# Kernel optimization log

Hardware: AMD Instinct MI355X
Metric: run time of the kernel (lower is better)

## Reference

```python
import jax, jax.numpy as jnp
import numpy as np

B, K, C, HEADS, R, N, FF = 8, 512, 256, 8, 4, 64, 1024
HT = 2 * R + 1  # rel-pos table side = 9


def layer_norm(x, g, b, eps=1e-5):
    mu = jnp.mean(x, axis=-1, keepdims=True)
    var = jnp.var(x, axis=-1, keepdims=True)
    return (x - mu) * jax.lax.rsqrt(var + eps) * g + b


def grid_sample_table(table, grid):
    """Bilinear grid_sample, align_corners=True, zeros padding.
    table: [heads, H, W] (batch-expanded in torch, identical per batch)
    grid:  [b, k, n, 2] in [-1, 1]  ->  out [b, heads, k, n]
    """
    heads, H, W = table.shape
    gx = (grid[..., 0] + 1.0) * 0.5 * (W - 1)
    gy = (grid[..., 1] + 1.0) * 0.5 * (H - 1)
    x0 = jnp.floor(gx); y0 = jnp.floor(gy)
    x1 = x0 + 1.0;      y1 = y0 + 1.0
    wx1 = gx - x0; wx0 = 1.0 - wx1
    wy1 = gy - y0; wy0 = 1.0 - wy1
    flat = table.reshape(heads, H * W)

    def corner(yi, xi, w):
        valid = (xi >= 0) & (xi <= W - 1) & (yi >= 0) & (yi <= H - 1)
        idx = (jnp.clip(yi, 0, H - 1) * W + jnp.clip(xi, 0, W - 1)).astype(jnp.int32)
        return flat[:, idx] * jnp.where(valid, w, 0.0)[None]  # [heads,b,k,n]

    out = (corner(y0, x0, wy0 * wx0) + corner(y0, x1, wy0 * wx1)
           + corner(y1, x0, wy1 * wx0) + corner(y1, x1, wy1 * wx1))
    return jnp.moveaxis(out, 0, 1)  # [b, heads, k, n]


def setup_inputs() -> dict:
    key = jax.random.key(0)
    ks = jax.random.split(key, 16)
    s = 1.0 / np.sqrt(C)
    inp = {
        "query": jax.random.normal(ks[0], (B, K, C), jnp.float32),
        "local_feat": jax.random.normal(ks[1], (B, C, K, N), jnp.float32),
        "local_spat": jax.random.uniform(ks[2], (B, K, N, 2), jnp.float32) * 2.0 - 1.0,
        # rel-pos table is zeros-initialized in torch; use small randn so it's non-trivial
        "rel_table": jax.random.normal(ks[3], (HEADS, HT, HT), jnp.float32) * 0.02,
        "Wq": jax.random.normal(ks[4], (C, C), jnp.float32) * s,
        "bq": jnp.zeros((C,), jnp.float32),
        "Wk": jax.random.normal(ks[5], (C, C), jnp.float32) * s,
        "bk": jnp.zeros((C,), jnp.float32),
        "Wv": jax.random.normal(ks[6], (C, C), jnp.float32) * s,
        "bv": jnp.zeros((C,), jnp.float32),
        "Wo": jax.random.normal(ks[7], (C, C), jnp.float32) * s,
        "bo": jnp.zeros((C,), jnp.float32),
        "ln1_g": jnp.ones((C,), jnp.float32),
        "ln1_b": jnp.zeros((C,), jnp.float32),
        "W1": jax.random.normal(ks[8], (C, FF), jnp.float32) * s,
        "b1": jnp.zeros((FF,), jnp.float32),
        "W2": jax.random.normal(ks[9], (FF, C), jnp.float32) * (1.0 / np.sqrt(FF)),
        "b2": jnp.zeros((C,), jnp.float32),
        "ln2_g": jnp.ones((C,), jnp.float32),
        "ln2_b": jnp.zeros((C,), jnp.float32),
    }
    return inp


def reference(query, local_feat, local_spat, rel_table, Wq, bq, Wk, bk, Wv, bv,
              Wo, bo, ln1_g, ln1_b, W1, b1, W2, b2, ln2_g, ln2_b):
    b, k, c = query.shape
    heads = rel_table.shape[0]
    d = c // heads
    n = local_feat.shape[-1]
    # spatial_score: grid_sample of rel-pos table at per-key offsets -> attention bias
    bias = grid_sample_table(rel_table, local_spat)      # [b, heads, k, n]
    bias = jnp.transpose(bias, (0, 2, 1, 3))             # [b, k, heads, n]
    # local bilateral attention (query attends to its n local samples)
    q = (query @ Wq + bq).reshape(b, k, heads, d)
    feats = jnp.transpose(local_feat, (0, 2, 3, 1))      # [b, k, n, c]
    Kp = (feats @ Wk + bk).reshape(b, k, n, heads, d)
    Vp = (feats @ Wv + bv).reshape(b, k, n, heads, d)
    scores = jnp.einsum('bkhd,bknhd->bkhn', q, Kp) / jnp.sqrt(jnp.float32(d)) + bias
    attn = jax.nn.softmax(scores, axis=-1)
    ctx = jnp.einsum('bkhn,bknhd->bkhd', attn, Vp).reshape(b, k, c)
    x = layer_norm(query + ctx @ Wo + bo, ln1_g, ln1_b)
    h = jax.nn.gelu(x @ W1 + b1) @ W2 + b2
    out = layer_norm(x + h, ln2_g, ln2_b)
    # num_local_scales == 1: stack+mean over scales is identity
    return out
```

## Files before the change

kernel.cpp:

```cpp
#include <hip/hip_runtime.h>
#include <hip/hip_bf16.h>

typedef __hip_bfloat16 bf16;
typedef __attribute__((ext_vector_type(8))) short short8;
typedef __attribute__((ext_vector_type(4))) float float4_;

#define DEV static __device__ __forceinline__

DEV float blo(unsigned w){ return __uint_as_float(w << 16); }
DEV float bhi(unsigned w){ return __uint_as_float(w & 0xffff0000u); }
DEV unsigned short f2bu(float x){ bf16 h = __float2bfloat16(x); unsigned short u; __builtin_memcpy(&u, &h, 2); return u; }
DEV unsigned pack2(float a, float b){ return (unsigned)f2bu(a) | ((unsigned)f2bu(b) << 16); }

DEV float gelu_tanh(float x){
  float z = 0.7978845608028654f * (x + 0.044715f * x * x * x);
  float th = 2.0f / (1.0f + __expf(-2.0f * z)) - 1.0f;
  return 0.5f * x * (1.0f + th);
}


__global__ __launch_bounds__(256) void k_prep(
    const float* __restrict__ query, const float* __restrict__ Wq,
    const float* __restrict__ Wk, const float* __restrict__ Wv,
    const float* __restrict__ Wo, const float* __restrict__ W1, const float* __restrict__ W2,
    bf16* __restrict__ query_bf, bf16* __restrict__ WqT, bf16* __restrict__ WkP,
    bf16* __restrict__ WvP, bf16* __restrict__ WoT, bf16* __restrict__ W1T, bf16* __restrict__ W2T)
{
  __shared__ ushort ts[64][72];
  const int t = threadIdx.x;
  const int bx = blockIdx.x;

  if (bx < 160){
    const float* src; bf16* dst; int ldi, ldo, kt, nt;
    if (bx < 16)      { src = Wq; dst = WqT; ldi = 256;  ldo = 256;  kt = bx & 3;        nt = bx >> 2; }
    else if (bx < 32) { src = Wo; dst = WoT; ldi = 256;  ldo = 256;  kt = (bx-16) & 3;   nt = (bx-16) >> 2; }
    else if (bx < 96) { src = W1; dst = W1T; ldi = 1024; ldo = 256;  kt = (bx-32) & 3;   nt = (bx-32) >> 2; }
    else              { src = W2; dst = W2T; ldi = 256;  ldo = 1024; kt = (bx-96) & 15;  nt = (bx-96) >> 4; }
    int k0 = kt * 64, n0 = nt * 64;
    {
      int r = t >> 2, c0 = (t & 3) * 16;
      #pragma unroll
      for (int g = 0; g < 4; g++){
        float4 v = *(const float4*)&src[(size_t)(k0 + r)*ldi + n0 + c0 + g*4];
        ts[r][c0+g*4+0] = f2bu(v.x); ts[r][c0+g*4+1] = f2bu(v.y);
        ts[r][c0+g*4+2] = f2bu(v.z); ts[r][c0+g*4+3] = f2bu(v.w);
      }
    }
    __syncthreads();
    {
      int rr = t >> 2, cc0 = (t & 3) * 16;
      unsigned wbuf[8];
      #pragma unroll
      for (int j = 0; j < 8; j++)
        wbuf[j] = (unsigned)ts[cc0+2*j][rr] | ((unsigned)ts[cc0+2*j+1][rr] << 16);
      uint4* d = (uint4*)(dst + (size_t)(n0 + rr)*ldo + k0 + cc0);
      d[0] = make_uint4(wbuf[0], wbuf[1], wbuf[2], wbuf[3]);
      d[1] = make_uint4(wbuf[4], wbuf[5], wbuf[6], wbuf[7]);
    }
  } else if (bx < 192){
    int idx = bx - 160, h = idx >> 2, kt = idx & 3, k0 = kt * 64;
    {
      int r = t >> 2, d0 = (t & 3) * 8;
      #pragma unroll
      for (int g = 0; g < 2; g++){
        float4 v = *(const float4*)&Wv[(size_t)(k0 + r)*256 + h*32 + d0 + g*4];
        ts[r][d0+g*4+0] = f2bu(v.x); ts[r][d0+g*4+1] = f2bu(v.y);
        ts[r][d0+g*4+2] = f2bu(v.z); ts[r][d0+g*4+3] = f2bu(v.w);
      }
    }
    __syncthreads();
    {
      int d = t >> 3, cc0 = (t & 7) * 8;
      unsigned wbuf[4];
      #pragma unroll
      for (int j = 0; j < 4; j++)
        wbuf[j] = (unsigned)ts[cc0+2*j][d] | ((unsigned)ts[cc0+2*j+1][d] << 16);
      *(uint4*)(WvP + (size_t)h*8192 + (size_t)d*256 + k0 + cc0) =
          make_uint4(wbuf[0], wbuf[1], wbuf[2], wbuf[3]);
    }
  } else if (bx < 200){
    int off = (bx - 192) * 8192;
    #pragma unroll
    for (int g = 0; g < 8; g++){
      int i = off + g*1024 + t*4;
      int h = i >> 13, c = (i >> 5) & 255, d = i & 31;
      float4 v = *(const float4*)&Wk[(size_t)c*256 + h*32 + d];
      *(uint2*)(WkP + i) = make_uint2(pack2(v.x, v.y), pack2(v.z, v.w));
    }
  } else {
    int off = (bx - 200) * 16384;
    #pragma unroll
    for (int g = 0; g < 16; g++){
      int i = off + g*1024 + t*4;
      float4 v = *(const float4*)&query[i];
      *(uint2*)(query_bf + i) = make_uint2(pack2(v.x, v.y), pack2(v.z, v.w));
    }
  }
}

template<int KDIM, int NT, int EPI>
__global__ __launch_bounds__(256) void k_gemm(
    const bf16* __restrict__ A, int lda, int acolH,
    const bf16* __restrict__ BT, int btH,
    const float* __restrict__ bias,
    bf16* __restrict__ Cb, int ldc, int ncolH)
{
  constexpr int KB = (KDIM >= 64) ? 64 : 32;
  constexpr int LP = KB + 8;
  constexpr int ASEG = KB / 8;
  __shared__ short As[64][LP];
  __shared__ short Bs[NT][LP];

  const int t = threadIdx.x;
  const int w = t >> 6, l = t & 63, lm = l & 15, lq = l >> 4;
  const int m0 = blockIdx.x * 64;
  const int h = blockIdx.z;
  const size_t acol = (size_t)h * acolH;
  const bf16* Bt = BT + (size_t)h * btH + (size_t)(blockIdx.y * NT) * KDIM;
  const int ncol = h * ncolH + blockIdx.y * NT;

  float4_ acc[NT/16];
  #pragma unroll
  for (int i = 0; i < NT/16; i++) acc[i] = (float4_){0.f,0.f,0.f,0.f};

  for (int k0 = 0; k0 < KDIM; k0 += KB){
    if (k0) __syncthreads();
    for (int i = t; i < 64*ASEG; i += 256){
      int row = i / ASEG, seg = i % ASEG;
      uint4 v = *(const uint4*)(A + (size_t)(m0+row)*lda + acol + k0 + seg*8);
      *(uint4*)&As[row][seg*8] = v;
    }
    for (int i = t; i < NT*ASEG; i += 256){
      int row = i / ASEG, seg = i % ASEG;
      uint4 v = *(const uint4*)(Bt + (size_t)row*KDIM + k0 + seg*8);
      *(uint4*)&Bs[row][seg*8] = v;
    }
    __syncthreads();
    #pragma unroll
    for (int kk = 0; kk < KB/32; kk++){
      short8 af = *(const short8*)&As[w*16 + lm][kk*32 + lq*8];
      #pragma unroll
      for (int nt = 0; nt < NT/16; nt++){
        short8 bfr = *(const short8*)&Bs[nt*16 + lm][kk*32 + lq*8];
        acc[nt] = __builtin_amdgcn_mfma_f32_16x16x32_bf16(af, bfr, acc[nt], 0, 0, 0);
      }
    }
  }

  #pragma unroll
  for (int nt = 0; nt < NT/16; nt++){
    int gcol = ncol + nt*16 + lm;
    float bb = bias ? bias[gcol] : 0.0f;
    #pragma unroll
    for (int rg = 0; rg < 4; rg++){
      int row = m0 + w*16 + lq*4 + rg;
      float v = acc[nt][rg] + bb;
      if (EPI == 0) Cb[(size_t)row*ldc + gcol] = __float2bfloat16(v);
      else          Cb[(size_t)row*ldc + gcol] = __float2bfloat16(gelu_tanh(v));
    }
  }
}

template<int KDIM, int WRITE_BF>
__global__ __launch_bounds__(256) void k_gemm_ln(
    const bf16* __restrict__ A, int lda,
    const bf16* __restrict__ BT,
    const float* __restrict__ bias,
    const float* __restrict__ resid,
    const float* __restrict__ gamma, const float* __restrict__ beta,
    float* __restrict__ Cf, bf16* __restrict__ Cb)
{
  constexpr int KB = 64, LP = 72;
  __shared__ short As[16][LP];
  __shared__ short Bs[256][LP];
  __shared__ float2 part[4][16];

  const int t = threadIdx.x;
  const int w = t >> 6, l = t & 63, lm = l & 15, lq = l >> 4;
  const int m0 = blockIdx.x * 16;

  float4_ acc[4];
  #pragma unroll
  for (int i = 0; i < 4; i++) acc[i] = (float4_){0.f,0.f,0.f,0.f};

  for (int k0 = 0; k0 < KDIM; k0 += KB){
    if (k0) __syncthreads();
    if (t < 128){
      int row = t >> 3, seg = t & 7;
      uint4 v = *(const uint4*)(A + (size_t)(m0+row)*lda + k0 + seg*8);
      *(uint4*)&As[row][seg*8] = v;
    }
    for (int i = t; i < 2048; i += 256){
      int row = i >> 3, seg = i & 7;
      uint4 v = *(const uint4*)(BT + (size_t)row*KDIM + k0 + seg*8);
      *(uint4*)&Bs[row][seg*8] = v;
    }
    __syncthreads();
    #pragma unroll
    for (int kk = 0; kk < 2; kk++){
      short8 af = *(const short8*)&As[lm][kk*32 + lq*8];
      #pragma unroll
      for (int nt = 0; nt < 4; nt++){
        short8 bfr = *(const short8*)&Bs[w*64 + nt*16 + lm][kk*32 + lq*8];
        acc[nt] = __builtin_amdgcn_mfma_f32_16x16x32_bf16(af, bfr, acc[nt], 0, 0, 0);
      }
    }
  }

  float v[4][4];
  float s1[4] = {0,0,0,0}, s2[4] = {0,0,0,0};
  #pragma unroll
  for (int nt = 0; nt < 4; nt++){
    int col = w*64 + nt*16 + lm;
    float bb = bias[col];
    #pragma unroll
    for (int rg = 0; rg < 4; rg++){
      int row = m0 + lq*4 + rg;
      float x = acc[nt][rg] + bb + resid[(size_t)row*256 + col];
      v[nt][rg] = x;
      s1[rg] += x; s2[rg] += x*x;
    }
  }
  #pragma unroll
  for (int off = 1; off < 16; off <<= 1){
    #pragma unroll
    for (int rg = 0; rg < 4; rg++){
      s1[rg] += __shfl_xor(s1[rg], off);
      s2[rg] += __shfl_xor(s2[rg], off);
    }
  }
  if (lm == 0){
    #pragma unroll
    for (int rg = 0; rg < 4; rg++)
      part[w][lq*4 + rg] = make_float2(s1[rg], s2[rg]);
  }
  __syncthreads();
  #pragma unroll
  for (int rg = 0; rg < 4; rg++){
    int rl = lq*4 + rg;
    float S1 = part[0][rl].x + part[1][rl].x + part[2][rl].x + part[3][rl].x;
    float S2 = part[0][rl].y + part[1][rl].y + part[2][rl].y + part[3][rl].y;
    float mean = S1 * (1.0f/256.0f);
    float var  = S2 * (1.0f/256.0f) - mean*mean;
    float inv  = rsqrtf(var + 1e-5f);
    #pragma unroll
    for (int nt = 0; nt < 4; nt++){
      int col = w*64 + nt*16 + lm;
      float o = (v[nt][rg] - mean) * inv * gamma[col] + beta[col];
      size_t idx = (size_t)(m0 + rl)*256 + col;
      Cf[idx] = o;
      if (WRITE_BF) Cb[idx] = __float2bfloat16(o);
    }
  }
}

__global__ __launch_bounds__(256) void k_attn(
    const float* __restrict__ local_feat, const float* __restrict__ local_spat,
    const float* __restrict__ rel_table, const bf16* __restrict__ qk,
    bf16* __restrict__ fctx)
{
  __shared__ __attribute__((aligned(16))) ushort fsT[64][264];
  __shared__ __attribute__((aligned(16))) ushort qkb[8][264];
  __shared__ float biasS[8][68];
  __shared__ float s_sc[64][10];
  __shared__ float attn_t[64][12];

  const int t = threadIdx.x;
  const int r = blockIdx.x;
  const int b = r >> 9, k = r & 511;
  const int w = t >> 6, l = t & 63, lm = l & 15, lq = l >> 4;

  {
    int cb = t >> 2;
    int nq = (t & 3) * 16;
    int key = (t & 3) << 3;
    #pragma unroll
    for (int p = 0; p < 4; p++){
      int c = p * 64 + cb;
      int cs = c ^ key;
      const float4* src = (const float4*)(local_feat + ((size_t)((b*256 + c)*512 + k))*64 + nq);
      #pragma unroll
      for (int g = 0; g < 4; g++){
        float4 v = src[g];
        int row = nq + g*4;
        fsT[row+0][cs] = f2bu(v.x);
        fsT[row+1][cs] = f2bu(v.y);
        fsT[row+2][cs] = f2bu(v.z);
        fsT[row+3][cs] = f2bu(v.w);
      }
    }
  }
  {
    uint4 a = *(const uint4*)(qk + (size_t)r * 2048 + t * 8);
    int h = t >> 5, c0 = (t & 31) * 8;
    *(uint4*)&qkb[h][c0] = a;
  }
  if (t < 64){
    float2 sxy = *(const float2*)&local_spat[((size_t)r*64 + t)*2];
    float gx = (sxy.x + 1.0f) * 4.0f, gy = (sxy.y + 1.0f) * 4.0f;
    float x0f = floorf(gx), y0f = floorf(gy);
    int xi0 = (int)x0f, yi0 = (int)y0f;
    float wx1 = gx - x0f, wx0 = 1.0f - wx1;
    float wy1 = gy - y0f, wy0 = 1.0f - wy1;
    int xs[4] = {xi0, xi0 + 1, xi0, xi0 + 1};
    int ys[4] = {yi0, yi0, yi0 + 1, yi0 + 1};
    float wj[4] = {wy0*wx0, wy0*wx1, wy1*wx0, wy1*wx1};
    float ww[4]; int ix[4];
    #pragma unroll
    for (int j = 0; j < 4; j++){
      bool valid = (xs[j] >= 0) && (xs[j] <= 8) && (ys[j] >= 0) && (ys[j] <= 8);
      ix[j] = min(max(ys[j],0),8)*9 + min(max(xs[j],0),8);
      ww[j] = valid ? wj[j] : 0.0f;
    }
    #pragma unroll
    for (int h = 0; h < 8; h++){
      const float* th = rel_table + h*81;
      biasS[h][t] = th[ix[0]]*ww[0] + th[ix[1]]*ww[1] + th[ix[2]]*ww[2] + th[ix[3]]*ww[3];
    }
  }
  __syncthreads();

  {
    float4_ acc = (float4_){0.f,0.f,0.f,0.f};
    const int skey = (w & 3) << 3;
    #pragma unroll
    for (int ks = 0; ks < 8; ks++){
      short8 af  = *(const short8*)&fsT[w*16 + lm][(ks*32 + lq*8) ^ skey];
      short8 bfr = *(const short8*)&qkb[lm & 7][ks*32 + lq*8];
      acc = __builtin_amdgcn_mfma_f32_16x16x32_bf16(af, bfr, acc, 0, 0, 0);
    }
    if (lm < 8){
      const float scale = 0.17677669529663687f;
      #pragma unroll
      for (int rg = 0; rg < 4; rg++){
        int n = w*16 + lq*4 + rg;
        s_sc[n][lm] = acc[rg] * scale + biasS[lm][n];
      }
    }
  }
  __syncthreads();

  {
    int g = t >> 5, j = t & 31;
    float sc0 = s_sc[j][g], sc1 = s_sc[j+32][g];
    float m = fmaxf(sc0, sc1);
    #pragma unroll
    for (int off = 1; off < 32; off <<= 1) m = fmaxf(m, __shfl_xor(m, off));
    float e0 = __expf(sc0 - m), e1 = __expf(sc1 - m);
    float s = e0 + e1;
    #pragma unroll
    for (int off = 1; off < 32; off <<= 1) s += __shfl_xor(s, off);
    float inv = 1.0f / s;
    attn_t[j][g]    = e0 * inv;
    attn_t[j+32][g] = e1 * inv;
  }
  __syncthreads();

  {
    const int cg = t >> 2, hh = t & 3;
    const int c0 = cg * 4, h0 = hh * 2;
    float f0[4] = {0,0,0,0}, f1[4] = {0,0,0,0};
    #pragma unroll 4
    for (int n = 0; n < 64; n++){
      int key = ((n >> 4) & 3) << 3;
      uint2 wv = *(const uint2*)&fsT[n][c0 ^ key];
      float a0 = blo(wv.x), a1 = bhi(wv.x), a2 = blo(wv.y), a3 = bhi(wv.y);
      float2 A = *(const float2*)&attn_t[n][h0];
      f0[0] += A.x*a0; f0[1] += A.x*a1; f0[2] += A.x*a2; f0[3] += A.x*a3;
      f1[0] += A.y*a0; f1[1] += A.y*a1; f1[2] += A.y*a2; f1[3] += A.y*a3;
    }
    size_t base = (size_t)r*2048 + (size_t)h0*256 + c0;
    *(uint2*)&fctx[base]       = make_uint2(pack2(f0[0], f0[1]), pack2(f0[2], f0[3]));
    *(uint2*)&fctx[base + 256] = make_uint2(pack2(f1[0], f1[1]), pack2(f1[2], f1[3]));
  }
}

extern "C" void kernel_launch(void* const* d_in, const int* in_sizes, int n_in,
                              void* d_out, int out_size, void* d_ws, size_t ws_size,
                              hipStream_t stream)
{
  const float* query      = (const float*)d_in[0];
  const float* local_feat = (const float*)d_in[1];
  const float* local_spat = (const float*)d_in[2];
  const float* rel_table  = (const float*)d_in[3];
  const float* Wq  = (const float*)d_in[4];   const float* bq  = (const float*)d_in[5];
  const float* Wk  = (const float*)d_in[6];
  const float* Wv  = (const float*)d_in[8];   const float* bv  = (const float*)d_in[9];
  const float* Wo  = (const float*)d_in[10];  const float* bo  = (const float*)d_in[11];
  const float* g1  = (const float*)d_in[12];  const float* be1 = (const float*)d_in[13];
  const float* W1  = (const float*)d_in[14];  const float* b1  = (const float*)d_in[15];
  const float* W2  = (const float*)d_in[16];  const float* b2  = (const float*)d_in[17];
  const float* g2  = (const float*)d_in[18];  const float* be2 = (const float*)d_in[19];

  char* ws = (char*)d_ws;
  bf16*  qk       = (bf16*)(ws + 0);
  bf16*  fctx     = (bf16*)(ws + 16777216);
  bf16*  query_bf = (bf16*)(ws + 33554432);
  bf16*  q_bf     = (bf16*)(ws + 35651584);
  bf16*  WqT      = (bf16*)(ws + 37748736);
  bf16*  WkP      = (bf16*)(ws + 37879808);
  bf16*  WvP      = (bf16*)(ws + 38010880);
  bf16*  WoT      = (bf16*)(ws + 38141952);
  bf16*  W1T      = (bf16*)(ws + 38273024);
  bf16*  W2T      = (bf16*)(ws + 38797312);
  bf16*  ctx_bf   = (bf16*)(ws + 0);
  float* x        = (float*)(ws + 2097152);
  bf16*  x_bf     = (bf16*)(ws + 6291456);
  bf16*  h1       = (bf16*)(ws + 20971520);
  float* out      = (float*)d_out;

  dim3 blk(256);
  k_prep<<<dim3(264), blk, 0, stream>>>(query, Wq, Wk, Wv, Wo, W1, W2,
                                        query_bf, WqT, WkP, WvP, WoT, W1T, W2T);
  k_gemm<256,64,0><<<dim3(64,4,1), blk, 0, stream>>>(query_bf, 256, 0, WqT, 0, bq, q_bf, 256, 0);
  k_gemm<32,64,0><<<dim3(64,4,8), blk, 0, stream>>>(q_bf, 256, 32, WkP, 8192, nullptr, qk, 2048, 256);
  k_attn<<<dim3(4096), blk, 0, stream>>>(local_feat, local_spat, rel_table, qk, fctx);
  k_gemm<256,32,0><<<dim3(64,1,8), blk, 0, stream>>>(fctx, 2048, 256, WvP, 8192, bv, ctx_bf, 256, 32);
  k_gemm_ln<256,1><<<dim3(256), blk, 0, stream>>>(ctx_bf, 256, WoT, bo, query, g1, be1, x, x_bf);
  k_gemm<256,64,2><<<dim3(64,16,1), blk, 0, stream>>>(x_bf, 256, 0, W1T, 0, b1, h1, 1024, 0);
  k_gemm_ln<1024,0><<<dim3(256), blk, 0, stream>>>(h1, 1024, W2T, b2, x, g2, be2, out, nullptr);
}
```

Baseline: 504.0 us.

## Compute attention-weighted feature sum with MFMA using a second transposed LDS copy

The per-head weighted sum over the 64 local samples moves from scalar FMA loops to bf16 MFMA. To feed it, the features are stored in LDS twice, in [n][c] and [c][n] layouts, each with XOR swizzles. The loads now use wider vector stores, the scores are kept head-major, and the attention probabilities are rounded to bf16. This trades more LDS footprint and one extra bf16 rounding of the probabilities for fewer ALU instructions and fewer LDS reads in the attention kernel.

Measured after the change: 502.1 us, median of 2. No clear change (-0.4%).

```diff
diff --git a/kernel.cpp b/kernel.cpp
--- a/kernel.cpp
+++ b/kernel.cpp
@@ -259,11 +259,12 @@
     const float* __restrict__ rel_table, const bf16* __restrict__ qk,
     bf16* __restrict__ fctx)
 {
-  __shared__ __attribute__((aligned(16))) ushort fsT[64][264];
-  __shared__ __attribute__((aligned(16))) ushort qkb[8][264];
-  __shared__ float biasS[8][68];
-  __shared__ float s_sc[64][10];
-  __shared__ float attn_t[64][12];
+  __shared__ __attribute__((aligned(16))) ushort fsT[64][256];
+  __shared__ __attribute__((aligned(16))) ushort fs[256][64];
+  __shared__ __attribute__((aligned(16))) ushort qkb[8][272];
+  __shared__ __attribute__((aligned(16))) ushort attnT[16][64];
+  __shared__ __attribute__((aligned(16))) float biasS[8][68];
+  __shared__ __attribute__((aligned(16))) float s_scT[8][68];
 
   const int t = threadIdx.x;
   const int r = blockIdx.x;
@@ -271,22 +272,36 @@
   const int w = t >> 6, l = t & 63, lm = l & 15, lq = l >> 4;
 
   {
-    int cb = t >> 2;
-    int nq = (t & 3) * 16;
-    int key = (t & 3) << 3;
+    const int cpair = t >> 3;
+    const int mrow  = t & 7;
+    const int nq8   = mrow * 8;
     #pragma unroll
     for (int p = 0; p < 4; p++){
-      int c = p * 64 + cb;
-      int cs = c ^ key;
-      const float4* src = (const float4*)(local_feat + ((size_t)((b*256 + c)*512 + k))*64 + nq);
-      #pragma unroll
-      for (int g = 0; g < 4; g++){
-        float4 v = src[g];
-        int row = nq + g*4;
-        fsT[row+0][cs] = f2bu(v.x);
-        fsT[row+1][cs] = f2bu(v.y);
-        fsT[row+2][cs] = f2bu(v.z);
-        fsT[row+3][cs] = f2bu(v.w);
+      int c0 = p*64 + cpair*2, c1 = c0 + 1;
+      const float* s0 = local_feat + ((size_t)((b*256 + c0)*512 + k))*64 + nq8;
+      const float* s1 = local_feat + ((size_t)((b*256 + c1)*512 + k))*64 + nq8;
+      float4 a0 = *(const float4*)(s0);
+      float4 a1 = *(const float4*)(s0 + 4);
+      float4 b0 = *(const float4*)(s1);
+      float4 b1 = *(const float4*)(s1 + 4);
+      ushort u0[8] = { f2bu(a0.x), f2bu(a0.y), f2bu(a0.z), f2bu(a0.w),
+                       f2bu(a1.x), f2bu(a1.y), f2bu(a1.z), f2bu(a1.w) };
+      ushort u1[8] = { f2bu(b0.x), f2bu(b0.y), f2bu(b0.z), f2bu(b0.w),
+                       f2bu(b1.x), f2bu(b1.y), f2bu(b1.z), f2bu(b1.w) };
+      {
+        int sw0 = nq8 ^ ((c0 & 7) << 3);
+        int sw1 = nq8 ^ ((c1 & 7) << 3);
+        *(uint4*)&fs[c0][sw0] = make_uint4(
+            (unsigned)u0[0] | ((unsigned)u0[1]<<16), (unsigned)u0[2] | ((unsigned)u0[3]<<16),
+            (unsigned)u0[4] | ((unsigned)u0[5]<<16), (unsigned)u0[6] | ((unsigned)u0[7]<<16));
+        *(uint4*)&fs[c1][sw1] = make_uint4(
+            (unsigned)u1[0] | ((unsigned)u1[1]<<16), (unsigned)u1[2] | ((unsigned)u1[3]<<16),
+            (unsigned)u1[4] | ((unsigned)u1[5]<<16), (unsigned)u1[6] | ((unsigned)u1[7]<<16));
+      }
+      #pragma unroll
+      for (int i = 0; i < 8; i++){
+        int key = ((mrow ^ i) & 7) << 3;
+        *(unsigned*)&fsT[nq8 + i][c0 ^ key] = (unsigned)u0[i] | ((unsigned)u1[i] << 16);
       }
     }
   }
@@ -322,27 +337,30 @@
 
   {
     float4_ acc = (float4_){0.f,0.f,0.f,0.f};
-    const int skey = (w & 3) << 3;
+    const int arow = w*16 + lm;
+    const int akey = (((arow >> 3) ^ arow) & 7) << 3;
     #pragma unroll
     for (int ks = 0; ks < 8; ks++){
-      short8 af  = *(const short8*)&fsT[w*16 + lm][(ks*32 + lq*8) ^ skey];
+      short8 af  = *(const short8*)&fsT[arow][(ks*32 + lq*8) ^ akey];
       short8 bfr = *(const short8*)&qkb[lm & 7][ks*32 + lq*8];
       acc = __builtin_amdgcn_mfma_f32_16x16x32_bf16(af, bfr, acc, 0, 0, 0);
     }
     if (lm < 8){
       const float scale = 0.17677669529663687f;
-      #pragma unroll
-      for (int rg = 0; rg < 4; rg++){
-        int n = w*16 + lq*4 + rg;
-        s_sc[n][lm] = acc[rg] * scale + biasS[lm][n];
-      }
+      int n0 = w*16 + lq*4;
+      float4 sv;
+      sv.x = acc[0]*scale + biasS[lm][n0+0];
+      sv.y = acc[1]*scale + biasS[lm][n0+1];
+      sv.z = acc[2]*scale + biasS[lm][n0+2];
+      sv.w = acc[3]*scale + biasS[lm][n0+3];
+      *(float4*)&s_scT[lm][n0] = sv;
     }
   }
   __syncthreads();
 
   {
     int g = t >> 5, j = t & 31;
-    float sc0 = s_sc[j][g], sc1 = s_sc[j+32][g];
+    float sc0 = s_scT[g][j], sc1 = s_scT[g][j+32];
     float m = fmaxf(sc0, sc1);
     #pragma unroll
     for (int off = 1; off < 32; off <<= 1) m = fmaxf(m, __shfl_xor(m, off));
@@ -351,27 +369,34 @@
     #pragma unroll
     for (int off = 1; off < 32; off <<= 1) s += __shfl_xor(s, off);
     float inv = 1.0f / s;
-    attn_t[j][g]    = e0 * inv;
-    attn_t[j+32][g] = e1 * inv;
+    ushort p0 = f2bu(e0 * inv), p1 = f2bu(e1 * inv);
+    int key = g << 3;
+    attnT[g    ][j        ^ key] = p0;
+    attnT[g    ][(j + 32) ^ key] = p1;
+    attnT[g + 8][j        ^ key] = p0;
+    attnT[g + 8][(j + 32) ^ key] = p1;
   }
   __syncthreads();
 
   {
-    const int cg = t >> 2, hh = t & 3;
-    const int c0 = cg * 4, h0 = hh * 2;
-    float f0[4] = {0,0,0,0}, f1[4] = {0,0,0,0};
-    #pragma unroll 4
-    for (int n = 0; n < 64; n++){
-      int key = ((n >> 4) & 3) << 3;
-      uint2 wv = *(const uint2*)&fsT[n][c0 ^ key];
-      float a0 = blo(wv.x), a1 = bhi(wv.x), a2 = blo(wv.y), a3 = bhi(wv.y);
-      float2 A = *(const float2*)&attn_t[n][h0];
-      f0[0] += A.x*a0; f0[1] += A.x*a1; f0[2] += A.x*a2; f0[3] += A.x*a3;
-      f1[0] += A.y*a0; f1[1] += A.y*a1; f1[2] += A.y*a2; f1[3] += A.y*a3;
-    }
-    size_t base = (size_t)r*2048 + (size_t)h0*256 + c0;
-    *(uint2*)&fctx[base]       = make_uint2(pack2(f0[0], f0[1]), pack2(f0[2], f0[3]));
-    *(uint2*)&fctx[base + 256] = make_uint2(pack2(f1[0], f1[1]), pack2(f1[2], f1[3]));
+    const int bkey = (lm & 7) << 3;
+    short8 bf0 = *(const short8*)&attnT[lm][(      lq*8) ^ bkey];
+    short8 bf1 = *(const short8*)&attnT[lm][(32 + lq*8) ^ bkey];
+    #pragma unroll
+    for (int ct = 0; ct < 4; ct++){
+      int crow = (w*4 + ct)*16 + lm;
+      int ckey = (crow & 7) << 3;
+      float4_ acc2 = (float4_){0.f,0.f,0.f,0.f};
+      short8 af0 = *(const short8*)&fs[crow][(      lq*8) ^ ckey];
+      acc2 = __builtin_amdgcn_mfma_f32_16x16x32_bf16(af0, bf0, acc2, 0, 0, 0);
+      short8 af1 = *(const short8*)&fs[crow][(32 + lq*8) ^ ckey];
+      acc2 = __builtin_amdgcn_mfma_f32_16x16x32_bf16(af1, bf1, acc2, 0, 0, 0);
+      if (lm < 8){
+        int c = (w*4 + ct)*16 + lq*4;
+        size_t base = (size_t)r*2048 + (size_t)lm*256 + c;
+        *(uint2*)&fctx[base] = make_uint2(pack2(acc2[0], acc2[1]), pack2(acc2[2], acc2[3]));
+      }
+    }
   }
 }
 
```
